# Kernel tuning notes

Measured on AMD Instinct MI355X. Metric: run time of the kernel, lower is better.

The kernel has to match this reference:

```python
import jax, jax.numpy as jnp
import numpy as np

N_HEAD = 8
QKV_DIM = 64
EMBED = 128
MASK_FILL = 1e-10  # module uses masked_fill_ with 1e-10, not -inf
LN_EPS = 1e-5


def setup_inputs() -> dict:
    key = jax.random.key(0)
    k1, k2, k3, k4, k5, k6 = jax.random.split(key, 6)
    B, S = 4, 2048
    inputQ = jax.random.normal(k1, (B, S, EMBED), dtype=jnp.float32)
    inputK = jax.random.normal(k2, (B, S, EMBED), dtype=jnp.float32)
    inputV = jax.random.normal(k3, (B, S, EMBED), dtype=jnp.float32)
    self_attention_mask = jax.random.randint(k4, (B, S, S), 0, 2).astype(bool)
    # Linear weights (torch layout: [out_features, in_features], no bias)
    WQ = jax.random.normal(k5, (N_HEAD * QKV_DIM, EMBED), dtype=jnp.float32) * 0.02
    Wfc = jax.random.normal(k6, (EMBED, N_HEAD * QKV_DIM), dtype=jnp.float32) * 0.02
    return {"inputQ": inputQ, "inputK": inputK, "inputV": inputV,
            "WQ": WQ, "Wfc": Wfc, "self_attention_mask": self_attention_mask}


def reference(inputQ, inputK, inputV, WQ, Wfc, self_attention_mask):
    B, S, E = inputQ.shape
    H, D = N_HEAD, QKV_DIM
    # Faithful to source: WQ is used for Q, K, and V; raw reshape (no transpose)
    Q = (inputQ @ WQ.T).reshape(B, H, -1, D)  # [B,H,S,D]
    K = (inputK @ WQ.T).reshape(B, H, -1, D)
    V = (inputV @ WQ.T).reshape(B, H, -1, D)
    scores = jnp.einsum('bhqd,bhkd->bhqk', Q, K)  # no 1/sqrt(d) scaling in source
    scores = jnp.where(self_attention_mask[:, None, :, :], MASK_FILL, scores)
    attn = jax.nn.softmax(scores, axis=-1)
    Z = jnp.einsum('bhqk,bhkd->bhqd', attn, V)
    self_attn_out = Z.reshape(B, -1, H * D) @ Wfc.T  # [B,S,E]
    x = inputQ + self_attn_out
    # fresh nn.LayerNorm: weight=1, bias=0, eps=1e-5
    mu = jnp.mean(x, axis=-1, keepdims=True)
    var = jnp.var(x, axis=-1, keepdims=True)
    return (x - mu) * jax.lax.rsqrt(var + LN_EPS)
```

## Files before the change

kernel.cpp:

```cpp
#include <hip/hip_runtime.h>

typedef short s16x8 __attribute__((ext_vector_type(8)));
typedef float f32x4 __attribute__((ext_vector_type(4)));
typedef unsigned short u16;
typedef unsigned int u32;
typedef unsigned long long u64;

#define MFMA16(A,B,C) __builtin_amdgcn_mfma_f32_16x16x32_bf16(A,B,C,0,0,0)


__device__ __forceinline__ u16 f2bf(float f){
  union { float f; u32 u; } v; v.f = f;
  u32 r = v.u + 0x7fffu + ((v.u >> 16) & 1u);
  return (u16)(r >> 16);
}

__device__ __forceinline__ s16x8 pack8(float4 a, float4 b){
  s16x8 o;
  o[0]=(short)f2bf(a.x); o[1]=(short)f2bf(a.y); o[2]=(short)f2bf(a.z); o[3]=(short)f2bf(a.w);
  o[4]=(short)f2bf(b.x); o[5]=(short)f2bf(b.y); o[6]=(short)f2bf(b.z); o[7]=(short)f2bf(b.w);
  return o;
}

__global__ void detect_mask_kernel(const u32* __restrict__ mask, int* __restrict__ flag){
  u32 v = mask[threadIdx.x];
  u64 b = __ballot(v <= 1u);
  if (threadIdx.x == 0) *flag = (b == ~0ull) ? 1 : 0;
}

__global__ __launch_bounds__(256) void pack_mask_kernel(const void* __restrict__ mask,
                                                        u64* __restrict__ bits,
                                                        const int* __restrict__ flag){
  int w = blockIdx.x * 256 + threadIdx.x;
  u64 out = 0;
  if (*flag) {
    const int4* p = (const int4*)mask + (size_t)w * 16;
    #pragma unroll
    for (int i = 0; i < 16; i++){
      int4 v = p[i];
      out |= (u64)(v.x != 0) << (i*4+0);
      out |= (u64)(v.y != 0) << (i*4+1);
      out |= (u64)(v.z != 0) << (i*4+2);
      out |= (u64)(v.w != 0) << (i*4+3);
    }
  } else {
    const uint4* p = (const uint4*)mask + (size_t)w * 4;
    #pragma unroll
    for (int i = 0; i < 4; i++){
      uint4 v = p[i];
      u32 ws_[4] = {v.x, v.y, v.z, v.w};
      #pragma unroll
      for (int j = 0; j < 4; j++){
        #pragma unroll
        for (int e = 0; e < 4; e++)
          out |= (u64)((ws_[j] >> (8*e)) & 1u) << (i*16 + j*4 + e);
      }
    }
  }
  bits[w] = out;
}

__global__ __launch_bounds__(256) void qkv_proj_kernel(const float* __restrict__ X,
                                                       const float* __restrict__ Wq,
                                                       u16* __restrict__ P){
  int mt  = blockIdx.x >> 3;
  int nt2 = blockIdx.x & 7;
  int tid = threadIdx.x, wv = tid >> 6, lane = tid & 63, g = lane >> 4, c = lane & 15;
  int m0 = mt * 128 + wv * 32;
  int n0 = nt2 * 64;

  f32x4 acc[2][4];
  #pragma unroll
  for (int i = 0; i < 2; i++)
    #pragma unroll
    for (int j = 0; j < 4; j++){ f32x4 z = {0.f,0.f,0.f,0.f}; acc[i][j] = z; }

  #pragma unroll
  for (int ks = 0; ks < 4; ks++){
    int kk = ks * 32 + g * 8;
    s16x8 a[2], bb[4];
    #pragma unroll
    for (int mi = 0; mi < 2; mi++){
      const float* ap = X + (size_t)(m0 + mi*16 + c) * 128 + kk;
      a[mi] = pack8(*(const float4*)ap, *(const float4*)(ap + 4));
    }
    #pragma unroll
    for (int ni = 0; ni < 4; ni++){
      const float* bp = Wq + (size_t)(n0 + ni*16 + c) * 128 + kk;
      bb[ni] = pack8(*(const float4*)bp, *(const float4*)(bp + 4));
    }
    #pragma unroll
    for (int mi = 0; mi < 2; mi++)
      #pragma unroll
      for (int ni = 0; ni < 4; ni++)
        acc[mi][ni] = MFMA16(a[mi], bb[ni], acc[mi][ni]);
  }
  #pragma unroll
  for (int mi = 0; mi < 2; mi++)
    #pragma unroll
    for (int ni = 0; ni < 4; ni++)
      #pragma unroll
      for (int r = 0; r < 4; r++){
        int row = m0 + mi*16 + g*4 + r;
        int col = n0 + ni*16 + c;
        P[(size_t)row * 512 + col] = f2bf(acc[mi][ni][r]);
      }
}

__global__ __launch_bounds__(256) void transpose_v_kernel(const u16* __restrict__ Pv,
                                                          u16* __restrict__ VT){
  int bh = blockIdx.x >> 6;
  int ch = blockIdx.x & 63;
  int lane = threadIdx.x & 63, wv = threadIdx.x >> 6;
  const u16* V = Pv + (size_t)bh * 131072;
  u16* T = VT + (size_t)bh * 131072;
  int kbase = ch * 32 + wv * 8;
  s16x8 o;
  #pragma unroll
  for (int j = 0; j < 8; j++)
    o[j] = (short)V[(size_t)(kbase + j) * 64 + lane];
  *(s16x8*)&T[(size_t)lane * 2048 + kbase] = o;
}

__global__ __launch_bounds__(256, 2) void attn_kernel(const u16* __restrict__ Pq,
                                                      const u16* __restrict__ Pk,
                                                      const u16* __restrict__ VT,
                                                      const u64* __restrict__ mbits,
                                                      u16* __restrict__ Z){
  __shared__ u16 plds[4][2048];
  int bid0 = blockIdx.x;
  int bid = (bid0 & 7)*64 + (bid0 >> 3);
  int bh = bid >> 4, qt = bid & 15;
  int b = bh >> 3;
  int tid = threadIdx.x, wv = tid >> 6, lane = tid & 63, g = lane >> 4, c = lane & 15;
  const u16* Qh = Pq + (size_t)bh*131072;
  const u16* Kh = Pk + (size_t)bh*131072;
  const u16* Th = VT + (size_t)bh*131072;
  int q0w = qt*128 + wv*32;

  s16x8 aq[2][2];
  #pragma unroll
  for (int qt2=0; qt2<2; qt2++)
    #pragma unroll
    for (int h=0; h<2; h++)
      aq[qt2][h] = *(const s16x8*)&Qh[(size_t)(q0w+qt2*16+c)*64 + h*32 + g*8];

  const u64* mb = mbits + (size_t)(b*2048 + q0w)*32;

  s16x8 kb[4][2], vb[4][2];
  u64 mw[2][4];
  #pragma unroll
  for (int nt=0; nt<4; nt++)
    #pragma unroll
    for (int h=0; h<2; h++)
      kb[nt][h] = *(const s16x8*)&Kh[(size_t)(nt*16+c)*64 + h*32 + g*8];
  #pragma unroll
  for (int dt=0; dt<4; dt++)
    #pragma unroll
    for (int h=0; h<2; h++)
      vb[dt][h] = *(const s16x8*)&Th[(size_t)(dt*16+c)*2048 + h*32 + g*8];
  #pragma unroll
  for (int qt2=0; qt2<2; qt2++)
    #pragma unroll
    for (int r=0; r<4; r++)
      mw[qt2][r] = mb[(qt2*16+g*4+r)*32];

  f32x4 zac[2][4];
  #pragma unroll
  for (int i=0;i<2;i++)
    #pragma unroll
    for (int j=0;j<4;j++){ f32x4 z = {0.f,0.f,0.f,0.f}; zac[i][j]=z; }
  float den[2][4] = {{0.f,0.f,0.f,0.f},{0.f,0.f,0.f,0.f}};
  u16* pw = &plds[wv][0];
  int xc = (c&7)<<3;

  for (int t = 0; t < 32; t++){
    int tn = (t+1)&31;
    int kvn = tn*64;

    f32x4 s[2][4];
    #pragma unroll
    for (int qt2=0; qt2<2; qt2++)
      #pragma unroll
      for (int nt=0; nt<4; nt++){
        f32x4 sa = {0.f,0.f,0.f,0.f};
        sa = MFMA16(aq[qt2][0], kb[nt][0], sa);
        sa = MFMA16(aq[qt2][1], kb[nt][1], sa);
        s[qt2][nt] = sa;
      }
    #pragma unroll
    for (int nt=0; nt<4; nt++)
      #pragma unroll
      for (int h=0; h<2; h++)
        kb[nt][h] = *(const s16x8*)&Kh[(size_t)(kvn+nt*16+c)*64 + h*32 + g*8];

    #pragma unroll
    for (int qt2=0; qt2<2; qt2++)
      #pragma unroll
      for (int r=0; r<4; r++){
        int ql = qt2*16 + g*4 + r;
        int xr = ((g*4+r)&7) << 3;
        #pragma unroll
        for (int nt=0; nt<4; nt++){
          int kpos = nt*16 + c;
          float p = ((mw[qt2][r] >> kpos) & 1ull) ? 1.0f : __expf(s[qt2][nt][r]);
          den[qt2][r] += p;
          pw[ql*64 + (kpos ^ xr)] = f2bf(p);
        }
      }
    #pragma unroll
    for (int qt2=0; qt2<2; qt2++)
      #pragma unroll
      for (int r=0; r<4; r++)
        mw[qt2][r] = mb[(qt2*16+g*4+r)*32 + tn];

    #pragma unroll
    for (int qt2=0; qt2<2; qt2++){
      int qrow = qt2*16 + c;
      s16x8 ap0 = *(const s16x8*)&pw[qrow*64 + ((g*8) ^ xc)];
      s16x8 ap1 = *(const s16x8*)&pw[qrow*64 + ((32+g*8) ^ xc)];
      #pragma unroll
      for (int dt=0; dt<4; dt++){
        zac[qt2][dt] = MFMA16(ap0, vb[dt][0], zac[qt2][dt]);
        zac[qt2][dt] = MFMA16(ap1, vb[dt][1], zac[qt2][dt]);
      }
    }
    #pragma unroll
    for (int dt=0; dt<4; dt++)
      #pragma unroll
      for (int h=0; h<2; h++)
        vb[dt][h] = *(const s16x8*)&Th[(size_t)(dt*16+c)*2048 + kvn + h*32 + g*8];
  }

  #pragma unroll
  for (int qt2=0; qt2<2; qt2++)
    #pragma unroll
    for (int r=0; r<4; r++){
      float d = den[qt2][r];
      d += __shfl_xor(d, 1, 64);
      d += __shfl_xor(d, 2, 64);
      d += __shfl_xor(d, 4, 64);
      d += __shfl_xor(d, 8, 64);
      den[qt2][r] = 1.0f / d;
    }
  u16* Zh = Z + (size_t)bh*131072;
  #pragma unroll
  for (int qt2=0; qt2<2; qt2++)
    #pragma unroll
    for (int dt=0; dt<4; dt++)
      #pragma unroll
      for (int r=0; r<4; r++)
        Zh[(size_t)(q0w + qt2*16 + g*4 + r)*64 + dt*16 + c] = f2bf(zac[qt2][dt][r] * den[qt2][r]);
}

__global__ __launch_bounds__(256) void fc_ln_kernel(const u16* __restrict__ ZR,
                                                    const float* __restrict__ Wfc,
                                                    const float* __restrict__ Xq,
                                                    float* __restrict__ out){
  int tid = threadIdx.x, wv = tid >> 6, lane = tid & 63, g = lane >> 4, c = lane & 15;
  int m0 = blockIdx.x * 64 + wv * 16;

  f32x4 acc[8];
  #pragma unroll
  for (int i = 0; i < 8; i++){ f32x4 z = {0.f,0.f,0.f,0.f}; acc[i] = z; }

  for (int ks = 0; ks < 16; ks++){
    int kk = ks * 32 + g * 8;
    s16x8 a = *(const s16x8*)&ZR[(size_t)(m0 + c) * 512 + kk];
    #pragma unroll
    for (int nt = 0; nt < 8; nt++){
      const float* wp = &Wfc[(size_t)(nt*16 + c) * 512 + kk];
      s16x8 bb = pack8(*(const float4*)wp, *(const float4*)(wp + 4));
      acc[nt] = MFMA16(a, bb, acc[nt]);
    }
  }
  float xs[8][4];
  float sum[4] = {0.f,0.f,0.f,0.f}, ssq[4] = {0.f,0.f,0.f,0.f};
  #pragma unroll
  for (int r = 0; r < 4; r++){
    int row = m0 + g*4 + r;
    #pragma unroll
    for (int nt = 0; nt < 8; nt++){
      float x = acc[nt][r] + Xq[(size_t)row * 128 + nt*16 + c];
      xs[nt][r] = x; sum[r] += x; ssq[r] += x * x;
    }
  }
  #pragma unroll
  for (int r = 0; r < 4; r++){
    float s_ = sum[r], q_ = ssq[r];
    #pragma unroll
    for (int off = 1; off < 16; off <<= 1){
      s_ += __shfl_xor(s_, off, 64);
      q_ += __shfl_xor(q_, off, 64);
    }
    sum[r] = s_; ssq[r] = q_;
  }
  #pragma unroll
  for (int r = 0; r < 4; r++){
    int row = m0 + g*4 + r;
    float mean = sum[r] * (1.0f/128.0f);
    float var  = ssq[r] * (1.0f/128.0f) - mean * mean;
    float rstd = rsqrtf(var + 1e-5f);
    #pragma unroll
    for (int nt = 0; nt < 8; nt++)
      out[(size_t)row * 128 + nt*16 + c] = (xs[nt][r] - mean) * rstd;
  }
}

extern "C" void kernel_launch(void* const* d_in, const int* in_sizes, int n_in,
                              void* d_out, int out_size, void* d_ws, size_t ws_size,
                              hipStream_t stream) {
  const float* inQ  = (const float*)d_in[0];
  const float* inK  = (const float*)d_in[1];
  const float* inV  = (const float*)d_in[2];
  const float* WQ   = (const float*)d_in[3];
  const float* Wfc  = (const float*)d_in[4];
  const void*  mask = (const void*) d_in[5];
  float* out = (float*)d_out;

  char* ws = (char*)d_ws;
  int* flag  = (int*)ws;
  u64* mbits = (u64*)(ws + (1u << 20));
  u16* Pq    = (u16*)(ws + (4u  << 20));
  u16* Pk    = (u16*)(ws + (12u << 20));
  u16* Pv    = (u16*)(ws + (20u << 20));
  u16* VTb   = (u16*)(ws + (28u << 20));
  u16* Zb    = (u16*)(ws + (36u << 20));

  detect_mask_kernel<<<dim3(1), dim3(64), 0, stream>>>((const u32*)mask, flag);
  pack_mask_kernel<<<dim3(1024), dim3(256), 0, stream>>>(mask, mbits, flag);
  qkv_proj_kernel<<<dim3(512), dim3(256), 0, stream>>>(inQ, WQ, Pq);
  qkv_proj_kernel<<<dim3(512), dim3(256), 0, stream>>>(inK, WQ, Pk);
  qkv_proj_kernel<<<dim3(512), dim3(256), 0, stream>>>(inV, WQ, Pv);
  transpose_v_kernel<<<dim3(2048), dim3(256), 0, stream>>>(Pv, VTb);
  attn_kernel<<<dim3(512), dim3(256), 0, stream>>>(Pq, Pk, VTb, mbits, Zb);
  fc_ln_kernel<<<dim3(128), dim3(256), 0, stream>>>(Zb, Wfc, inQ, out);
}
```

Baseline: 365.4 us.

## Halve attention query tile per wave and pre-pack weights to bf16

```diff
diff --git a/kernel.cpp b/kernel.cpp
--- a/kernel.cpp
+++ b/kernel.cpp
@@ -60,8 +60,21 @@
   bits[w] = out;
 }
 
+__global__ __launch_bounds__(256) void pack_w_kernel(const float* __restrict__ WQ,
+                                                     const float* __restrict__ Wfc,
+                                                     u16* __restrict__ WQb,
+                                                     u16* __restrict__ Wfcb){
+  int bid = blockIdx.x;
+  const float* src = (bid < 32) ? WQ  : Wfc;
+  u16*        dst = (bid < 32) ? WQb : Wfcb;
+  size_t off = (size_t)(bid & 31)*2048 + (size_t)threadIdx.x*8;
+  float4 a = *(const float4*)(src+off);
+  float4 b = *(const float4*)(src+off+4);
+  *(s16x8*)(dst+off) = pack8(a,b);
+}
+
 __global__ __launch_bounds__(256) void qkv_proj_kernel(const float* __restrict__ X,
-                                                       const float* __restrict__ Wq,
+                                                       const u16* __restrict__ Wb,
                                                        u16* __restrict__ P){
   int mt  = blockIdx.x >> 3;
   int nt2 = blockIdx.x & 7;
@@ -85,10 +98,8 @@
       a[mi] = pack8(*(const float4*)ap, *(const float4*)(ap + 4));
     }
     #pragma unroll
-    for (int ni = 0; ni < 4; ni++){
-      const float* bp = Wq + (size_t)(n0 + ni*16 + c) * 128 + kk;
-      bb[ni] = pack8(*(const float4*)bp, *(const float4*)(bp + 4));
-    }
+    for (int ni = 0; ni < 4; ni++)
+      bb[ni] = *(const s16x8*)&Wb[(size_t)(n0 + ni*16 + c) * 128 + kk];
     #pragma unroll
     for (int mi = 0; mi < 2; mi++)
       #pragma unroll
@@ -122,33 +133,31 @@
   *(s16x8*)&T[(size_t)lane * 2048 + kbase] = o;
 }
 
-__global__ __launch_bounds__(256, 2) void attn_kernel(const u16* __restrict__ Pq,
+__global__ __launch_bounds__(256, 4) void attn_kernel(const u16* __restrict__ Pq,
                                                       const u16* __restrict__ Pk,
                                                       const u16* __restrict__ VT,
                                                       const u64* __restrict__ mbits,
                                                       u16* __restrict__ Z){
-  __shared__ u16 plds[4][2048];
+  __shared__ u16 plds[4][1024];
   int bid0 = blockIdx.x;
-  int bid = (bid0 & 7)*64 + (bid0 >> 3);
-  int bh = bid >> 4, qt = bid & 15;
+  int bid = (bid0 & 7)*128 + (bid0 >> 3);
+  int bh = bid >> 5, qt = bid & 31;
   int b = bh >> 3;
   int tid = threadIdx.x, wv = tid >> 6, lane = tid & 63, g = lane >> 4, c = lane & 15;
   const u16* Qh = Pq + (size_t)bh*131072;
   const u16* Kh = Pk + (size_t)bh*131072;
   const u16* Th = VT + (size_t)bh*131072;
-  int q0w = qt*128 + wv*32;
-
-  s16x8 aq[2][2];
-  #pragma unroll
-  for (int qt2=0; qt2<2; qt2++)
-    #pragma unroll
-    for (int h=0; h<2; h++)
-      aq[qt2][h] = *(const s16x8*)&Qh[(size_t)(q0w+qt2*16+c)*64 + h*32 + g*8];
+  int q0w = qt*64 + wv*16;
+
+  s16x8 aq[2];
+  #pragma unroll
+  for (int h=0; h<2; h++)
+    aq[h] = *(const s16x8*)&Qh[(size_t)(q0w+c)*64 + h*32 + g*8];
 
   const u64* mb = mbits + (size_t)(b*2048 + q0w)*32;
 
   s16x8 kb[4][2], vb[4][2];
-  u64 mw[2][4];
+  u64 mw[4];
   #pragma unroll
   for (int nt=0; nt<4; nt++)
     #pragma unroll
@@ -160,17 +169,13 @@
     for (int h=0; h<2; h++)
       vb[dt][h] = *(const s16x8*)&Th[(size_t)(dt*16+c)*2048 + h*32 + g*8];
   #pragma unroll
-  for (int qt2=0; qt2<2; qt2++)
-    #pragma unroll
-    for (int r=0; r<4; r++)
-      mw[qt2][r] = mb[(qt2*16+g*4+r)*32];
-
-  f32x4 zac[2][4];
-  #pragma unroll
-  for (int i=0;i<2;i++)
-    #pragma unroll
-    for (int j=0;j<4;j++){ f32x4 z = {0.f,0.f,0.f,0.f}; zac[i][j]=z; }
-  float den[2][4] = {{0.f,0.f,0.f,0.f},{0.f,0.f,0.f,0.f}};
+  for (int r=0; r<4; r++)
+    mw[r] = mb[(g*4+r)*32];
+
+  f32x4 zac[4];
+  #pragma unroll
+  for (int j=0;j<4;j++){ f32x4 z = {0.f,0.f,0.f,0.f}; zac[j]=z; }
+  float den[4] = {0.f,0.f,0.f,0.f};
   u16* pw = &plds[wv][0];
   int xc = (c&7)<<3;
 
@@ -178,16 +183,14 @@
     int tn = (t+1)&31;
     int kvn = tn*64;
 
-    f32x4 s[2][4];
-    #pragma unroll
-    for (int qt2=0; qt2<2; qt2++)
-      #pragma unroll
-      for (int nt=0; nt<4; nt++){
-        f32x4 sa = {0.f,0.f,0.f,0.f};
-        sa = MFMA16(aq[qt2][0], kb[nt][0], sa);
-        sa = MFMA16(aq[qt2][1], kb[nt][1], sa);
-        s[qt2][nt] = sa;
-      }
+    f32x4 s[4];
+    #pragma unroll
+    for (int nt=0; nt<4; nt++){
+      f32x4 sa = {0.f,0.f,0.f,0.f};
+      sa = MFMA16(aq[0], kb[nt][0], sa);
+      sa = MFMA16(aq[1], kb[nt][1], sa);
+      s[nt] = sa;
+    }
     #pragma unroll
     for (int nt=0; nt<4; nt++)
       #pragma unroll
@@ -195,34 +198,28 @@
         kb[nt][h] = *(const s16x8*)&Kh[(size_t)(kvn+nt*16+c)*64 + h*32 + g*8];
 
     #pragma unroll
-    for (int qt2=0; qt2<2; qt2++)
-      #pragma unroll
-      for (int r=0; r<4; r++){
-        int ql = qt2*16 + g*4 + r;
-        int xr = ((g*4+r)&7) << 3;
-        #pragma unroll
-        for (int nt=0; nt<4; nt++){
-          int kpos = nt*16 + c;
-          float p = ((mw[qt2][r] >> kpos) & 1ull) ? 1.0f : __expf(s[qt2][nt][r]);
-          den[qt2][r] += p;
-          pw[ql*64 + (kpos ^ xr)] = f2bf(p);
-        }
+    for (int r=0; r<4; r++){
+      int ql = g*4 + r;
+      int xr = (ql&7) << 3;
+      #pragma unroll
+      for (int nt=0; nt<4; nt++){
+        int kpos = nt*16 + c;
+        float p = ((mw[r] >> kpos) & 1ull) ? 1.0f : __expf(s[nt][r]);
+        den[r] += p;
+        pw[ql*64 + (kpos ^ xr)] = f2bf(p);
       }
-    #pragma unroll
-    for (int qt2=0; qt2<2; qt2++)
-      #pragma unroll
-      for (int r=0; r<4; r++)
-        mw[qt2][r] = mb[(qt2*16+g*4+r)*32 + tn];
-
-    #pragma unroll
-    for (int qt2=0; qt2<2; qt2++){
-      int qrow = qt2*16 + c;
-      s16x8 ap0 = *(const s16x8*)&pw[qrow*64 + ((g*8) ^ xc)];
-      s16x8 ap1 = *(const s16x8*)&pw[qrow*64 + ((32+g*8) ^ xc)];
+    }
+    #pragma unroll
+    for (int r=0; r<4; r++)
+      mw[r] = mb[(g*4+r)*32 + tn];
+
+    {
+      s16x8 ap0 = *(const s16x8*)&pw[c*64 + ((g*8) ^ xc)];
+      s16x8 ap1 = *(const s16x8*)&pw[c*64 + ((32+g*8) ^ xc)];
       #pragma unroll
       for (int dt=0; dt<4; dt++){
-        zac[qt2][dt] = MFMA16(ap0, vb[dt][0], zac[qt2][dt]);
-        zac[qt2][dt] = MFMA16(ap1, vb[dt][1], zac[qt2][dt]);
+        zac[dt] = MFMA16(ap0, vb[dt][0], zac[dt]);
+        zac[dt] = MFMA16(ap1, vb[dt][1], zac[dt]);
       }
     }
     #pragma unroll
@@ -233,28 +230,24 @@
   }
 
   #pragma unroll
-  for (int qt2=0; qt2<2; qt2++)
-    #pragma unroll
-    for (int r=0; r<4; r++){
-      float d = den[qt2][r];
-      d += __shfl_xor(d, 1, 64);
-      d += __shfl_xor(d, 2, 64);
-      d += __shfl_xor(d, 4, 64);
-      d += __shfl_xor(d, 8, 64);
-      den[qt2][r] = 1.0f / d;
-    }
+  for (int r=0; r<4; r++){
+    float d = den[r];
+    d += __shfl_xor(d, 1, 64);
+    d += __shfl_xor(d, 2, 64);
+    d += __shfl_xor(d, 4, 64);
+    d += __shfl_xor(d, 8, 64);
+    den[r] = 1.0f / d;
+  }
   u16* Zh = Z + (size_t)bh*131072;
   #pragma unroll
-  for (int qt2=0; qt2<2; qt2++)
-    #pragma unroll
-    for (int dt=0; dt<4; dt++)
-      #pragma unroll
-      for (int r=0; r<4; r++)
-        Zh[(size_t)(q0w + qt2*16 + g*4 + r)*64 + dt*16 + c] = f2bf(zac[qt2][dt][r] * den[qt2][r]);
+  for (int dt=0; dt<4; dt++)
+    #pragma unroll
+    for (int r=0; r<4; r++)
+      Zh[(size_t)(q0w + g*4 + r)*64 + dt*16 + c] = f2bf(zac[dt][r] * den[r]);
 }
 
 __global__ __launch_bounds__(256) void fc_ln_kernel(const u16* __restrict__ ZR,
-                                                    const float* __restrict__ Wfc,
+                                                    const u16* __restrict__ Wfcb,
                                                     const float* __restrict__ Xq,
                                                     float* __restrict__ out){
   int tid = threadIdx.x, wv = tid >> 6, lane = tid & 63, g = lane >> 4, c = lane & 15;
@@ -269,8 +262,7 @@
     s16x8 a = *(const s16x8*)&ZR[(size_t)(m0 + c) * 512 + kk];
     #pragma unroll
     for (int nt = 0; nt < 8; nt++){
-      const float* wp = &Wfc[(size_t)(nt*16 + c) * 512 + kk];
-      s16x8 bb = pack8(*(const float4*)wp, *(const float4*)(wp + 4));
+      s16x8 bb = *(const s16x8*)&Wfcb[(size_t)(nt*16 + c) * 512 + kk];
       acc[nt] = MFMA16(a, bb, acc[nt]);
     }
   }
@@ -321,6 +313,8 @@
   char* ws = (char*)d_ws;
   int* flag  = (int*)ws;
   u64* mbits = (u64*)(ws + (1u << 20));
+  u16* WQb   = (u16*)(ws + (3u << 20));
+  u16* Wfcb  = (u16*)(ws + (3u << 20) + (128u << 10));
   u16* Pq    = (u16*)(ws + (4u  << 20));
   u16* Pk    = (u16*)(ws + (12u << 20));
   u16* Pv    = (u16*)(ws + (20u << 20));
@@ -329,10 +323,11 @@
 
   detect_mask_kernel<<<dim3(1), dim3(64), 0, stream>>>((const u32*)mask, flag);
   pack_mask_kernel<<<dim3(1024), dim3(256), 0, stream>>>(mask, mbits, flag);
-  qkv_proj_kernel<<<dim3(512), dim3(256), 0, stream>>>(inQ, WQ, Pq);
-  qkv_proj_kernel<<<dim3(512), dim3(256), 0, stream>>>(inK, WQ, Pk);
-  qkv_proj_kernel<<<dim3(512), dim3(256), 0, stream>>>(inV, WQ, Pv);
+  pack_w_kernel<<<dim3(64), dim3(256), 0, stream>>>(WQ, Wfc, WQb, Wfcb);
+  qkv_proj_kernel<<<dim3(512), dim3(256), 0, stream>>>(inQ, WQb, Pq);
+  qkv_proj_kernel<<<dim3(512), dim3(256), 0, stream>>>(inK, WQb, Pk);
+  qkv_proj_kernel<<<dim3(512), dim3(256), 0, stream>>>(inV, WQb, Pv);
   transpose_v_kernel<<<dim3(2048), dim3(256), 0, stream>>>(Pv, VTb);
-  attn_kernel<<<dim3(512), dim3(256), 0, stream>>>(Pq, Pk, VTb, mbits, Zb);
-  fc_ln_kernel<<<dim3(128), dim3(256), 0, stream>>>(Zb, Wfc, inQ, out);
-}
+  attn_kernel<<<dim3(1024), dim3(256), 0, stream>>>(Pq, Pk, VTb, mbits, Zb);
+  fc_ln_kernel<<<dim3(128), dim3(256), 0, stream>>>(Zb, Wfcb, inQ, out);
+}
```

Result: slower. 416.7 us (+14.0%).

## Pre-pack weights to bf16, vectorize P stores with permuted V key order

Applied to the files above, without the earlier changes.

```diff
diff --git a/kernel.cpp b/kernel.cpp
--- a/kernel.cpp
+++ b/kernel.cpp
@@ -1,4 +1,5 @@
 #include <hip/hip_runtime.h>
+#include <hip/hip_bf16.h>
 
 typedef short s16x8 __attribute__((ext_vector_type(8)));
 typedef float f32x4 __attribute__((ext_vector_type(4)));
@@ -10,16 +11,24 @@
 
 
 __device__ __forceinline__ u16 f2bf(float f){
-  union { float f; u32 u; } v; v.f = f;
-  u32 r = v.u + 0x7fffu + ((v.u >> 16) & 1u);
-  return (u16)(r >> 16);
+  union { __hip_bfloat16 h; u16 u; } x;
+  x.h = __float2bfloat16(f);
+  return x.u;
+}
+
+__device__ __forceinline__ u32 pk2(float lo, float hi){
+  union { __hip_bfloat162 h; u32 u; } x;
+  x.h = __float22bfloat162_rn(make_float2(lo, hi));
+  return x.u;
 }
 
 __device__ __forceinline__ s16x8 pack8(float4 a, float4 b){
-  s16x8 o;
-  o[0]=(short)f2bf(a.x); o[1]=(short)f2bf(a.y); o[2]=(short)f2bf(a.z); o[3]=(short)f2bf(a.w);
-  o[4]=(short)f2bf(b.x); o[5]=(short)f2bf(b.y); o[6]=(short)f2bf(b.z); o[7]=(short)f2bf(b.w);
-  return o;
+  union { __hip_bfloat162 h[4]; s16x8 v; } u;
+  u.h[0] = __float22bfloat162_rn(make_float2(a.x, a.y));
+  u.h[1] = __float22bfloat162_rn(make_float2(a.z, a.w));
+  u.h[2] = __float22bfloat162_rn(make_float2(b.x, b.y));
+  u.h[3] = __float22bfloat162_rn(make_float2(b.z, b.w));
+  return u.v;
 }
 
 __global__ void detect_mask_kernel(const u32* __restrict__ mask, int* __restrict__ flag){
@@ -60,8 +69,21 @@
   bits[w] = out;
 }
 
+__global__ __launch_bounds__(256) void pack_w_kernel(const float* __restrict__ WQ,
+                                                     const float* __restrict__ Wfc,
+                                                     u16* __restrict__ WQb,
+                                                     u16* __restrict__ Wfcb){
+  int bid = blockIdx.x;
+  const float* src = (bid < 32) ? WQ  : Wfc;
+  u16*        dst = (bid < 32) ? WQb : Wfcb;
+  size_t off = (size_t)(bid & 31)*2048 + (size_t)threadIdx.x*8;
+  float4 a = *(const float4*)(src+off);
+  float4 b = *(const float4*)(src+off+4);
+  *(s16x8*)(dst+off) = pack8(a,b);
+}
+
 __global__ __launch_bounds__(256) void qkv_proj_kernel(const float* __restrict__ X,
-                                                       const float* __restrict__ Wq,
+                                                       const u16* __restrict__ Wb,
                                                        u16* __restrict__ P){
   int mt  = blockIdx.x >> 3;
   int nt2 = blockIdx.x & 7;
@@ -85,10 +107,8 @@
       a[mi] = pack8(*(const float4*)ap, *(const float4*)(ap + 4));
     }
     #pragma unroll
-    for (int ni = 0; ni < 4; ni++){
-      const float* bp = Wq + (size_t)(n0 + ni*16 + c) * 128 + kk;
-      bb[ni] = pack8(*(const float4*)bp, *(const float4*)(bp + 4));
-    }
+    for (int ni = 0; ni < 4; ni++)
+      bb[ni] = *(const s16x8*)&Wb[(size_t)(n0 + ni*16 + c) * 128 + kk];
     #pragma unroll
     for (int mi = 0; mi < 2; mi++)
       #pragma unroll
@@ -117,8 +137,11 @@
   int kbase = ch * 32 + wv * 8;
   s16x8 o;
   #pragma unroll
-  for (int j = 0; j < 8; j++)
-    o[j] = (short)V[(size_t)(kbase + j) * 64 + lane];
+  for (int j = 0; j < 8; j++){
+    int x = kbase + j;
+    int src = (x & ~63) | (((x & 3) << 4) | ((x & 63) >> 2));
+    o[j] = (short)V[(size_t)src * 64 + lane];
+  }
   *(s16x8*)&T[(size_t)lane * 2048 + kbase] = o;
 }
 
@@ -199,14 +222,17 @@
       #pragma unroll
       for (int r=0; r<4; r++){
         int ql = qt2*16 + g*4 + r;
-        int xr = ((g*4+r)&7) << 3;
-        #pragma unroll
-        for (int nt=0; nt<4; nt++){
-          int kpos = nt*16 + c;
-          float p = ((mw[qt2][r] >> kpos) & 1ull) ? 1.0f : __expf(s[qt2][nt][r]);
-          den[qt2][r] += p;
-          pw[ql*64 + (kpos ^ xr)] = f2bf(p);
-        }
+        int xr = (ql&7) << 3;
+        u64 m = mw[qt2][r];
+        float p0 = ((m >> (c     )) & 1ull) ? 1.0f : __expf(s[qt2][0][r]);
+        float p1 = ((m >> (c + 16)) & 1ull) ? 1.0f : __expf(s[qt2][1][r]);
+        float p2 = ((m >> (c + 32)) & 1ull) ? 1.0f : __expf(s[qt2][2][r]);
+        float p3 = ((m >> (c + 48)) & 1ull) ? 1.0f : __expf(s[qt2][3][r]);
+        den[qt2][r] += (p0 + p1) + (p2 + p3);
+        uint2 w;
+        w.x = pk2(p0, p1);
+        w.y = pk2(p2, p3);
+        *(uint2*)&pw[ql*64 + ((4*c) ^ xr)] = w;
       }
     #pragma unroll
     for (int qt2=0; qt2<2; qt2++)
@@ -254,7 +280,7 @@
 }
 
 __global__ __launch_bounds__(256) void fc_ln_kernel(const u16* __restrict__ ZR,
-                                                    const float* __restrict__ Wfc,
+                                                    const u16* __restrict__ Wfcb,
                                                     const float* __restrict__ Xq,
                                                     float* __restrict__ out){
   int tid = threadIdx.x, wv = tid >> 6, lane = tid & 63, g = lane >> 4, c = lane & 15;
@@ -269,8 +295,7 @@
     s16x8 a = *(const s16x8*)&ZR[(size_t)(m0 + c) * 512 + kk];
     #pragma unroll
     for (int nt = 0; nt < 8; nt++){
-      const float* wp = &Wfc[(size_t)(nt*16 + c) * 512 + kk];
-      s16x8 bb = pack8(*(const float4*)wp, *(const float4*)(wp + 4));
+      s16x8 bb = *(const s16x8*)&Wfcb[(size_t)(nt*16 + c) * 512 + kk];
       acc[nt] = MFMA16(a, bb, acc[nt]);
     }
   }
@@ -321,6 +346,8 @@
   char* ws = (char*)d_ws;
   int* flag  = (int*)ws;
   u64* mbits = (u64*)(ws + (1u << 20));
+  u16* WQb   = (u16*)(ws + (3u << 20));
+  u16* Wfcb  = (u16*)(ws + (3u << 20) + (128u << 10));
   u16* Pq    = (u16*)(ws + (4u  << 20));
   u16* Pk    = (u16*)(ws + (12u << 20));
   u16* Pv    = (u16*)(ws + (20u << 20));
@@ -329,10 +356,11 @@
 
   detect_mask_kernel<<<dim3(1), dim3(64), 0, stream>>>((const u32*)mask, flag);
   pack_mask_kernel<<<dim3(1024), dim3(256), 0, stream>>>(mask, mbits, flag);
-  qkv_proj_kernel<<<dim3(512), dim3(256), 0, stream>>>(inQ, WQ, Pq);
-  qkv_proj_kernel<<<dim3(512), dim3(256), 0, stream>>>(inK, WQ, Pk);
-  qkv_proj_kernel<<<dim3(512), dim3(256), 0, stream>>>(inV, WQ, Pv);
+  pack_w_kernel<<<dim3(64), dim3(256), 0, stream>>>(WQ, Wfc, WQb, Wfcb);
+  qkv_proj_kernel<<<dim3(512), dim3(256), 0, stream>>>(inQ, WQb, Pq);
+  qkv_proj_kernel<<<dim3(512), dim3(256), 0, stream>>>(inK, WQb, Pk);
+  qkv_proj_kernel<<<dim3(512), dim3(256), 0, stream>>>(inV, WQb, Pv);
   transpose_v_kernel<<<dim3(2048), dim3(256), 0, stream>>>(Pv, VTb);
   attn_kernel<<<dim3(512), dim3(256), 0, stream>>>(Pq, Pk, VTb, mbits, Zb);
-  fc_ln_kernel<<<dim3(128), dim3(256), 0, stream>>>(Zb, Wfc, inQ, out);
-}
+  fc_ln_kernel<<<dim3(128), dim3(256), 0, stream>>>(Zb, Wfcb, inQ, out);
+}
```

Result: faster. 308.4 us (-15.6%).
